# Optimization experiments

Measured on AMD Instinct MI355X. Metric: run time of the kernel, lower is better.

## Reference

```python
import jax, jax.numpy as jnp
import numpy as np

K = 9            # connections per output pixel
GA = 2           # global additional samples
RA = 2           # relative additional samples
VS = 4 + GA + RA # 2^rank neighbours + sampled
REGION = 12      # int(0.25 * 48) per spatial dim
MMULT = 0.1
MIN_SIGMA = 0.05
SIGMA_SCALE = 0.05
SIGMA_BOOST = 2.0


def setup_inputs() -> dict:
    key = jax.random.key(0)
    ks = jax.random.split(key, 8)
    b, cin, h, w = 8, 128, 48, 48
    cout = 256
    hidden = cin * 4

    def lin_init(k, fan_out, fan_in):
        bound = 1.0 / np.sqrt(fan_in)
        kw, kb = jax.random.split(k)
        W = jax.random.uniform(kw, (fan_out, fan_in), minval=-bound, maxval=bound, dtype=jnp.float32)
        bb = jax.random.uniform(kb, (fan_out,), minval=-bound, maxval=bound, dtype=jnp.float32)
        return W, bb

    x = jax.random.normal(ks[0], (b, cin, h, w), dtype=jnp.float32)
    W1, b1 = lin_init(ks[1], hidden, 2)          # toparams layer 1 (adaptive=False -> 2 coord inputs)
    W2, b2 = lin_init(ks[2], 3 * K, hidden)      # toparams layer 2 -> k means (2d) + k sigmas
    Wu, bu = lin_init(ks[3], cout, K * cin)      # unify linear
    gints = jax.random.randint(ks[4], (b, h, w, K, GA, 2), 0, h, dtype=jnp.int32)      # global samples (h==w)
    roff = jax.random.randint(ks[5], (b, h, w, K, RA, 2), 0, REGION, dtype=jnp.int32)  # relative offsets
    return {"x": x, "W1": W1, "b1": b1, "W2": W2, "b2": b2, "Wu": Wu, "bu": bu,
            "gints": gints, "roff": roff}


def reference(x, W1, b1, W2, b2, Wu, bu, gints, roff):
    b, c, h, w = x.shape
    s = jnp.array([h, w], dtype=x.dtype)                       # spatial range per dim
    s_int = jnp.array([h, w], dtype=jnp.int32)

    # normalized coordinate grid in [0,1], (h, w, 2) with [.,.,0]=row, [.,.,1]=col
    rows = jnp.arange(h, dtype=x.dtype) / (h - 1)
    cols = jnp.arange(w, dtype=x.dtype) / (w - 1)
    coords = jnp.stack(jnp.meshgrid(rows, cols, indexing='ij'), axis=-1)

    # hypernetwork: per-pixel coords -> K 2d mean offsets + K sigmas
    inp = jnp.broadcast_to(coords, (b, h, w, 2))
    hid = jax.nn.relu(inp @ W1.T + b1)
    params = hid @ W2.T + b2                                   # (b,h,w,3K)
    means_raw = params[..., :2 * K].reshape(b, h, w, K, 2)
    sig_raw = params[..., 2 * K:]                              # (b,h,w,K)

    # mids: inverse of the sigmoid scaling applied to the pixel's own coordinate
    pix = coords * (s - 1)                                     # pixel coordinates
    sc = pix / (s - 1) * 0.9999 + 0.00005
    mids = jnp.log(sc / (1.0 - sc))                            # (h,w,2)

    # transform_means: sigmoid -> [0, s-1]
    means = jax.nn.sigmoid(mids[None, :, :, None, :] + MMULT * means_raw) * (s - 1)  # (b,h,w,K,2)
    # transform_sigmas: softplus(. + boost) + min, per-dim scale, then sigma_scale
    sigmas = (jax.nn.softplus(sig_raw + SIGMA_BOOST) + MIN_SIGMA)[..., None] * s * SIGMA_SCALE  # (b,h,w,K,2)

    # ---- integer index generation (non-differentiable) ----
    fl = jnp.floor(jax.lax.stop_gradient(means)).astype(jnp.int32)   # (b,h,w,K,2)
    combos = jnp.array([[0, 0], [0, 1], [1, 0], [1, 1]], dtype=jnp.int32)
    neigh = fl[..., None, :] + combos                                 # (b,h,w,K,4,2)
    rel = fl[..., None, :] + roff - REGION // 2                       # (b,h,w,K,RA,2)
    ints = jnp.concatenate([neigh, gints, rel], axis=-2) % s_int      # (b,h,w,K,VS,2)

    # duplicate masking: zero any tuple that occurred earlier along VS
    eq = jnp.all(ints[..., :, None, :] == ints[..., None, :, :], axis=-1)  # (...,VS,VS)
    lower = jnp.tril(jnp.ones((VS, VS), dtype=bool), k=-1)
    dups = jnp.any(eq & lower, axis=-1)                               # (b,h,w,K,VS)

    # unnormalized gaussian densities of integer points under (means, sigmas)
    diff = (ints.astype(x.dtype) - means[..., None, :]) / sigmas[..., None, :]
    props = jnp.exp(-0.5 * jnp.sum(diff * diff, axis=-1))             # (b,h,w,K,VS)
    props = jnp.where(dups, jnp.zeros((), x.dtype), props)
    weights = props / jnp.sum(props, axis=-1, keepdims=True)          # mvalues are all-ones

    # irregular gather of input channel vectors at sampled pixels
    lin = ints[..., 0] * w + ints[..., 1]                             # (b,h,w,K,VS)
    flat = x.transpose(0, 2, 3, 1).reshape(b, h * w, c)
    feats = flat[jnp.arange(b)[:, None], lin.reshape(b, -1)]          # (b, h*w*K*VS, c)
    feats = feats.reshape(b, h, w, K, VS, c)

    feats = jnp.einsum('bhwkvc,bhwkv->bhwkc', feats, weights)         # weighted reduce over VS
    feats = feats.reshape(b, h, w, K * c)
    out = feats @ Wu.T + bu                                           # unify linear
    return out.transpose(0, 3, 1, 2)                                  # (b, cout, h, w)
```

## Files before the change

kernel.cpp:

```cpp
#include <hip/hip_runtime.h>
#include <hip/hip_bf16.h>
#include <hip/hip_fp16.h>

#define BB 8
#define CIN 128
#define HH 48
#define WW 48
#define HW 2304
#define KK 9
#define COUT 256
#define KC 1152
#define MM 18432
#define MT 32
#define SFP 136

#define LIGHT_BARRIER() asm volatile("s_waitcnt lgkmcnt(0)\n\ts_barrier" ::: "memory")

typedef short bf16x8_t __attribute__((ext_vector_type(8)));
typedef float f32x16_t __attribute__((ext_vector_type(16)));
typedef float f32x4_t  __attribute__((ext_vector_type(4)));

static __device__ __forceinline__ float b2f(short u) {
    union { unsigned int i; float f; } c;
    c.i = ((unsigned int)(unsigned short)u) << 16;
    return c.f;
}

__global__ __launch_bounds__(256) void prep_kernel(
    const float* __restrict__ x, __hip_bfloat16* __restrict__ xT,
    const float* __restrict__ Wu, bf16x8_t* __restrict__ Bp,
    const float* __restrict__ W1, const float* __restrict__ b1,
    const float* __restrict__ W2, const float* __restrict__ b2,
    float* __restrict__ means, float* __restrict__ sigmas, int* __restrict__ fls)
{
    int bid = blockIdx.x;
    int t = threadIdx.x;

    if (bid < 576) {
        __shared__ float tile[64][65];
        int ij0 = (bid % 36) * 64;
        int c0  = ((bid / 36) % 2) * 64;
        int b   = bid / 72;
        int ijl = t & 63, cl = t >> 6;
        #pragma unroll
        for (int i = 0; i < 16; i++) {
            int cc = i*4 + cl;
            tile[cc][ijl] = x[(size_t)(b*CIN + c0 + cc) * HW + ij0 + ijl];
        }
        __syncthreads();
        int cl2 = t & 63, ijl2 = t >> 6;
        #pragma unroll
        for (int i = 0; i < 16; i++) {
            int ij = i*4 + ijl2;
            xT[(size_t)(b*HW + ij0 + ij) * CIN + c0 + cl2] = __float2bfloat16(tile[cl2][ij]);
        }
    } else if (bid < 720) {
        int idx = (bid - 576) * 256 + t;
        int lane = idx & 63;
        int rest = idx >> 6;
        int s = rest % 72, g = rest / 72;
        int r = lane & 31, qq = lane >> 5;
        const float* src = Wu + (size_t)(g*32 + r) * KC + s*16 + qq*8;
        union { bf16x8_t v; __hip_bfloat16 h[8]; } o;
        #pragma unroll
        for (int j = 0; j < 8; j++) o.h[j] = __float2bfloat16(src[j]);
        Bp[idx] = o.v;
    } else {
        int wave = t >> 6, lane = t & 63;
        int p = (bid - 720) * 4 + wave;
        int iy = p / WW, ix = p % WW;
        float ryf = (float)iy / 47.0f;
        float rxf = (float)ix / 47.0f;
        double ry = (double)ryf, rx = (double)rxf;

        double h[8];
        #pragma unroll
        for (int jj = 0; jj < 8; jj++) {
            int j = lane*8 + jj;
            double v = ry * (double)W1[j*2+0] + rx * (double)W1[j*2+1] + (double)b1[j];
            h[jj] = v > 0.0 ? v : 0.0;
        }
        double par[27];
        #pragma unroll
        for (int o = 0; o < 27; o++) {
            const float4* w4 = (const float4*)(W2 + (size_t)o*512 + lane*8);
            float4 wa = w4[0], wb = w4[1];
            double s = (double)wa.x*h[0] + (double)wa.y*h[1]
                     + (double)wa.z*h[2] + (double)wa.w*h[3]
                     + (double)wb.x*h[4] + (double)wb.y*h[5]
                     + (double)wb.z*h[6] + (double)wb.w*h[7];
            par[o] = s;
        }
        #pragma unroll
        for (int o = 0; o < 27; o++) {
            #pragma unroll
            for (int d = 1; d < 64; d <<= 1)
                par[o] += __shfl_xor(par[o], d, 64);
            par[o] += (double)b2[o];
        }
        if (lane < KK) {
            int k = lane;
            double scy = ry * 0.9999 + 5e-05;
            double scx = rx * 0.9999 + 5e-05;
            double midy = log(scy / (1.0 - scy));
            double midx = log(scx / (1.0 - scx));
            double zy = midy + 0.1 * par[2*k+0];
            double zx = midx + 0.1 * par[2*k+1];
            double my = 47.0 / (1.0 + exp(-zy));
            double mx = 47.0 / (1.0 + exp(-zx));
            double sr = par[18 + k] + 2.0;
            double sp = (sr > 0.0 ? sr : 0.0) + log1p(exp(-fabs(sr)));
            double sg = (sp + 0.05) * 48.0 * 0.05;
            means[(p*KK + k)*2 + 0] = (float)my;
            means[(p*KK + k)*2 + 1] = (float)mx;
            sigmas[p*KK + k] = (float)sg;
            fls[(p*KK + k)*2 + 0] = (int)floor(my);
            fls[(p*KK + k)*2 + 1] = (int)floor(mx);
        }
    }
}

__global__ __launch_bounds__(512, 4) void fused_kernel(
    const float* __restrict__ means, const float* __restrict__ sigmas,
    const int* __restrict__ fls, const int* __restrict__ gints,
    const int* __restrict__ roff, const short* __restrict__ xT,
    const bf16x8_t* __restrict__ Bp, const float* __restrict__ bu,
    float* __restrict__ out)
{
    __shared__ unsigned int s_tap[KK*MT*8];
    __shared__ __align__(16) short s_feat[2][MT*SFP];

    int t = threadIdx.x;
    int b   = blockIdx.x & 7;
    int grp = blockIdx.x >> 3;
    int ij0 = grp * MT;
    int m0  = b * HW + ij0;

    if (t < KK*MT) {
        int p = t;
        int k = p >> 5, row = p & 31;
        int ij = ij0 + row;
        int bij = m0 + row;
        int fy = fls[(ij*KK + k)*2 + 0];
        int fx = fls[(ij*KK + k)*2 + 1];
        float my = means[(ij*KK + k)*2 + 0];
        float mx = means[(ij*KK + k)*2 + 1];
        float sg = sigmas[ij*KK + k];
        int lins[8]; float ws[8];
        #pragma unroll
        for (int v = 0; v < 8; v++) {
            int iy, ix;
            if (v < 4) {
                iy = fy + (v >> 1); ix = fx + (v & 1);
            } else if (v < 6) {
                int base = ((bij*KK + k)*2 + (v - 4)) * 2;
                iy = gints[base]; ix = gints[base + 1];
            } else {
                int base = ((bij*KK + k)*2 + (v - 6)) * 2;
                iy = fy + roff[base] - 6; ix = fx + roff[base + 1] - 6;
            }
            iy = ((iy % HH) + HH) % HH;
            ix = ((ix % WW) + WW) % WW;
            lins[v] = iy * WW + ix;
            float dy = ((float)iy - my) / sg;
            float dx = ((float)ix - mx) / sg;
            ws[v] = expf(-0.5f * (dy*dy + dx*dx));
        }
        #pragma unroll
        for (int v = 1; v < 8; v++) {
            bool dup = false;
            #pragma unroll
            for (int u = 0; u < 8; u++) if (u < v) dup = dup || (lins[u] == lins[v]);
            if (dup) ws[v] = 0.0f;
        }
        float sum = 0.0f;
        #pragma unroll
        for (int v = 0; v < 8; v++) sum += ws[v];
        float inv = 1.0f / sum;
        #pragma unroll
        for (int v = 0; v < 8; v++) {
            unsigned short hb = __half_as_ushort(__float2half(ws[v] * inv));
            s_tap[p*8+v] = ((unsigned int)lins[v] << 16) | (unsigned int)hb;
        }
    }
    LIGHT_BARRIER();

    const short* xb = xT + (size_t)b * (HW * CIN);
    int lane = t & 63, wave = t >> 6;
    int r = lane & 31, q = lane >> 5;
    int grow = t >> 4, gc0 = (t & 15) << 3;

    f32x16_t acc = {};

    for (int k = 0; k < KK; k++) {
        bf16x8_t tap[8];
        float    wgt[8];
        {
            const unsigned int* tp = &s_tap[(k*MT + grow)*8];
            #pragma unroll
            for (int v = 0; v < 8; v++) {
                unsigned int e = tp[v];
                wgt[v] = __half2float(__ushort_as_half((unsigned short)(e & 0xffffu)));
                tap[v] = *(const bf16x8_t*)(xb + (size_t)(e >> 16) * CIN + gc0);
            }
        }
        {
            float a0[8];
            #pragma unroll
            for (int j = 0; j < 8; j++) a0[j] = 0.0f;
            #pragma unroll
            for (int v = 0; v < 8; v++) {
                float w = wgt[v]; bf16x8_t d8 = tap[v];
                #pragma unroll
                for (int j = 0; j < 8; j++) a0[j] += w * b2f(d8[j]);
            }
            union { bf16x8_t v8; __hip_bfloat16 hh[8]; } o;
            #pragma unroll
            for (int j = 0; j < 8; j++) o.hh[j] = __float2bfloat16(a0[j]);
            *(bf16x8_t*)(&s_feat[k & 1][grow*SFP + gc0]) = o.v8;
        }
        LIGHT_BARRIER();
        {
            int base = (wave*72 + k*8)*64 + lane;
            const short* fb = s_feat[k & 1];
            #pragma unroll
            for (int si = 0; si < 8; si++) {
                bf16x8_t Bf = Bp[base + si*64];
                bf16x8_t a = *(const bf16x8_t*)(fb + r*SFP + si*16 + q*8);
                acc = __builtin_amdgcn_mfma_f32_32x32x16_bf16(a, Bf, acc, 0, 0, 0);
            }
        }
    }

    int n = wave*32 + r;
    float bv = bu[n];
    float* oc = out + ((size_t)b * COUT + n) * HW + ij0;
    #pragma unroll
    for (int g4 = 0; g4 < 4; g4++) {
        f32x4_t vv;
        vv[0] = acc[g4*4+0] + bv;
        vv[1] = acc[g4*4+1] + bv;
        vv[2] = acc[g4*4+2] + bv;
        vv[3] = acc[g4*4+3] + bv;
        *(f32x4_t*)(oc + g4*8 + q*4) = vv;
    }
}

extern "C" void kernel_launch(void* const* d_in, const int* in_sizes, int n_in,
                              void* d_out, int out_size, void* d_ws, size_t ws_size,
                              hipStream_t stream)
{
    const float* x   = (const float*)d_in[0];
    const float* W1  = (const float*)d_in[1];
    const float* b1  = (const float*)d_in[2];
    const float* W2  = (const float*)d_in[3];
    const float* b2  = (const float*)d_in[4];
    const float* Wu  = (const float*)d_in[5];
    const float* bu  = (const float*)d_in[6];
    const int* gints = (const int*)d_in[7];
    const int* roff  = (const int*)d_in[8];
    float* out = (float*)d_out;

    char* ws = (char*)d_ws;
    float* ws_means  = (float*)(ws + 0);
    float* ws_sigma  = (float*)(ws + 165888);
    int*   ws_fl     = (int*  )(ws + 248832);
    short* ws_xT     = (short*)(ws + 414720);
    bf16x8_t* ws_bp  = (bf16x8_t*)(ws + 5133312);

    prep_kernel<<<1296, 256, 0, stream>>>(x, (__hip_bfloat16*)ws_xT, Wu, ws_bp,
                                          W1, b1, W2, b2,
                                          ws_means, ws_sigma, ws_fl);
    fused_kernel<<<MM/MT, 512, 0, stream>>>(ws_means, ws_sigma, ws_fl, gints, roff,
                                            ws_xT, ws_bp, bu, out);
}
```

Measured before the change: 145.3 us.

## Gather two kernel taps per iteration across thread halves to halve barriers

The gather stage now splits the 512 threads into two halves, each building the weighted feature tile for a different tap k, so two taps are produced per loop iteration. Each thread handles 16 channels (two 16-byte loads per sample) instead of 8. The loop runs 5 times instead of 9, cutting block barriers roughly in half and raising the number of gather loads in flight per thread. The cost is double the shared-memory feature buffer, more registers per thread, and an odd final iteration in which half the threads sit idle.

Result: slower. 150.1 us (+3.3%).

```diff
diff --git a/kernel.cpp b/kernel.cpp
--- a/kernel.cpp
+++ b/kernel.cpp
@@ -13,6 +13,7 @@
 #define MM 18432
 #define MT 32
 #define SFP 136
+#define NP 5
 
 #define LIGHT_BARRIER() asm volatile("s_waitcnt lgkmcnt(0)\n\ts_barrier" ::: "memory")
 
@@ -128,7 +129,7 @@
     float* __restrict__ out)
 {
     __shared__ unsigned int s_tap[KK*MT*8];
-    __shared__ __align__(16) short s_feat[2][MT*SFP];
+    __shared__ __align__(16) short s_feat[2][2][MT*SFP];
 
     int t = threadIdx.x;
     int b   = blockIdx.x & 7;
@@ -188,46 +189,61 @@
     const short* xb = xT + (size_t)b * (HW * CIN);
     int lane = t & 63, wave = t >> 6;
     int r = lane & 31, q = lane >> 5;
-    int grow = t >> 4, gc0 = (t & 15) << 3;
+    int cpart = t >> 8;
+    int grow = (t >> 3) & 31;
+    int gc0 = (t & 7) << 4;
 
     f32x16_t acc = {};
 
-    for (int k = 0; k < KK; k++) {
-        bf16x8_t tap[8];
-        float    wgt[8];
-        {
-            const unsigned int* tp = &s_tap[(k*MT + grow)*8];
+    for (int p = 0; p < NP; p++) {
+        int kg = 2*p + cpart;
+        if (kg < KK) {
+            const unsigned int* tp = &s_tap[(kg*MT + grow)*8];
+            unsigned int e[8];
+            #pragma unroll
+            for (int v = 0; v < 8; v++) e[v] = tp[v];
+            bf16x8_t d0[8], d1[8];
             #pragma unroll
             for (int v = 0; v < 8; v++) {
-                unsigned int e = tp[v];
-                wgt[v] = __half2float(__ushort_as_half((unsigned short)(e & 0xffffu)));
-                tap[v] = *(const bf16x8_t*)(xb + (size_t)(e >> 16) * CIN + gc0);
-            }
-        }
-        {
-            float a0[8];
-            #pragma unroll
-            for (int j = 0; j < 8; j++) a0[j] = 0.0f;
+                const bf16x8_t* sp = (const bf16x8_t*)(xb + (size_t)(e[v] >> 16) * CIN + gc0);
+                d0[v] = sp[0];
+                d1[v] = sp[1];
+            }
+            float a0[16];
+            #pragma unroll
+            for (int j = 0; j < 16; j++) a0[j] = 0.0f;
             #pragma unroll
             for (int v = 0; v < 8; v++) {
-                float w = wgt[v]; bf16x8_t d8 = tap[v];
+                float w = __half2float(__ushort_as_half((unsigned short)(e[v] & 0xffffu)));
                 #pragma unroll
-                for (int j = 0; j < 8; j++) a0[j] += w * b2f(d8[j]);
-            }
-            union { bf16x8_t v8; __hip_bfloat16 hh[8]; } o;
-            #pragma unroll
-            for (int j = 0; j < 8; j++) o.hh[j] = __float2bfloat16(a0[j]);
-            *(bf16x8_t*)(&s_feat[k & 1][grow*SFP + gc0]) = o.v8;
+                for (int j = 0; j < 8; j++) {
+                    a0[j]   += w * b2f(d0[v][j]);
+                    a0[8+j] += w * b2f(d1[v][j]);
+                }
+            }
+            union { bf16x8_t v8; __hip_bfloat16 hh[8]; } o0, o1;
+            #pragma unroll
+            for (int j = 0; j < 8; j++) {
+                o0.hh[j] = __float2bfloat16(a0[j]);
+                o1.hh[j] = __float2bfloat16(a0[8+j]);
+            }
+            bf16x8_t* fd = (bf16x8_t*)(&s_feat[p & 1][cpart][grow*SFP + gc0]);
+            fd[0] = o0.v8;
+            fd[1] = o1.v8;
         }
         LIGHT_BARRIER();
-        {
-            int base = (wave*72 + k*8)*64 + lane;
-            const short* fb = s_feat[k & 1];
-            #pragma unroll
-            for (int si = 0; si < 8; si++) {
-                bf16x8_t Bf = Bp[base + si*64];
-                bf16x8_t a = *(const bf16x8_t*)(fb + r*SFP + si*16 + q*8);
-                acc = __builtin_amdgcn_mfma_f32_32x32x16_bf16(a, Bf, acc, 0, 0, 0);
+        #pragma unroll
+        for (int cc = 0; cc < 2; cc++) {
+            int k = 2*p + cc;
+            if (k < KK) {
+                const short* fb = s_feat[p & 1][cc];
+                int base = (wave*72 + k*8)*64 + lane;
+                #pragma unroll
+                for (int si = 0; si < 8; si++) {
+                    bf16x8_t Bf = Bp[base + si*64];
+                    bf16x8_t a = *(const bf16x8_t*)(fb + r*SFP + si*16 + q*8);
+                    acc = __builtin_amdgcn_mfma_f32_32x32x16_bf16(a, Bf, acc, 0, 0, 0);
+                }
             }
         }
     }
```

## Warp-specialize fused kernel into gather producers and MFMA consumers with LDS flags

Applied to the files above, without the earlier changes.

Splits the block into 8 gather waves that build per-tap weighted feature tiles and 4 MFMA waves that each handle two 32-column output slices. Shared-memory counters with a triple-buffered feature tile replace the per-tap block barriers, so gathers for later taps can overlap the matrix multiply of earlier ones. The block grows to 768 threads and each consumer wave holds two accumulators, which raises register pressure and adds spin-wait overhead. The launch bound (768, 6) may also not fit the requested occupancy.

Measured after the change: 147.6 us. Within noise of the previous version (+1.6%).

```diff
diff --git a/kernel.cpp b/kernel.cpp
--- a/kernel.cpp
+++ b/kernel.cpp
@@ -13,8 +13,6 @@
 #define MM 18432
 #define MT 32
 #define SFP 136
-
-#define LIGHT_BARRIER() asm volatile("s_waitcnt lgkmcnt(0)\n\ts_barrier" ::: "memory")
 
 typedef short bf16x8_t __attribute__((ext_vector_type(8)));
 typedef float f32x16_t __attribute__((ext_vector_type(16)));
@@ -120,7 +118,7 @@
     }
 }
 
-__global__ __launch_bounds__(512, 4) void fused_kernel(
+__global__ __launch_bounds__(768, 6) void fused_kernel(
     const float* __restrict__ means, const float* __restrict__ sigmas,
     const int* __restrict__ fls, const int* __restrict__ gints,
     const int* __restrict__ roff, const short* __restrict__ xT,
@@ -128,13 +126,17 @@
     float* __restrict__ out)
 {
     __shared__ unsigned int s_tap[KK*MT*8];
-    __shared__ __align__(16) short s_feat[2][MT*SFP];
+    __shared__ __align__(16) short s_feat[3][MT*SFP];
+    __shared__ int s_ready[KK];
+    __shared__ int s_done[KK];
 
     int t = threadIdx.x;
     int b   = blockIdx.x & 7;
     int grp = blockIdx.x >> 3;
     int ij0 = grp * MT;
     int m0  = b * HW + ij0;
+
+    if (t < KK) { s_ready[t] = 0; s_done[t] = 0; }
 
     if (t < KK*MT) {
         int p = t;
@@ -183,66 +185,85 @@
             s_tap[p*8+v] = ((unsigned int)lins[v] << 16) | (unsigned int)hb;
         }
     }
-    LIGHT_BARRIER();
-
-    const short* xb = xT + (size_t)b * (HW * CIN);
+    __syncthreads();
+
     int lane = t & 63, wave = t >> 6;
-    int r = lane & 31, q = lane >> 5;
-    int grow = t >> 4, gc0 = (t & 15) << 3;
-
-    f32x16_t acc = {};
-
-    for (int k = 0; k < KK; k++) {
-        bf16x8_t tap[8];
-        float    wgt[8];
-        {
+
+    if (wave < 8) {
+        const short* xb = xT + (size_t)b * (HW * CIN);
+        int grow = t >> 4, gc0 = (t & 15) << 3;
+        for (int k = 0; k < KK; k++) {
+            if (k >= 3) {
+                while (__hip_atomic_load(&s_done[k-3], __ATOMIC_ACQUIRE,
+                                         __HIP_MEMORY_SCOPE_WORKGROUP) < 4)
+                    __builtin_amdgcn_s_sleep(1);
+            }
             const unsigned int* tp = &s_tap[(k*MT + grow)*8];
+            unsigned int e[8];
+            #pragma unroll
+            for (int v = 0; v < 8; v++) e[v] = tp[v];
+            bf16x8_t tap[8];
+            #pragma unroll
+            for (int v = 0; v < 8; v++)
+                tap[v] = *(const bf16x8_t*)(xb + (size_t)(e[v] >> 16) * CIN + gc0);
+            float a0[8];
+            #pragma unroll
+            for (int j = 0; j < 8; j++) a0[j] = 0.0f;
             #pragma unroll
             for (int v = 0; v < 8; v++) {
-                unsigned int e = tp[v];
-                wgt[v] = __half2float(__ushort_as_half((unsigned short)(e & 0xffffu)));
-                tap[v] = *(const bf16x8_t*)(xb + (size_t)(e >> 16) * CIN + gc0);
-            }
-        }
-        {
-            float a0[8];
-            #pragma unroll
-            for (int j = 0; j < 8; j++) a0[j] = 0.0f;
-            #pragma unroll
-            for (int v = 0; v < 8; v++) {
-                float w = wgt[v]; bf16x8_t d8 = tap[v];
+                float w = __half2float(__ushort_as_half((unsigned short)(e[v] & 0xffffu)));
+                bf16x8_t d8 = tap[v];
                 #pragma unroll
                 for (int j = 0; j < 8; j++) a0[j] += w * b2f(d8[j]);
             }
             union { bf16x8_t v8; __hip_bfloat16 hh[8]; } o;
             #pragma unroll
             for (int j = 0; j < 8; j++) o.hh[j] = __float2bfloat16(a0[j]);
-            *(bf16x8_t*)(&s_feat[k & 1][grow*SFP + gc0]) = o.v8;
-        }
-        LIGHT_BARRIER();
-        {
-            int base = (wave*72 + k*8)*64 + lane;
-            const short* fb = s_feat[k & 1];
-            #pragma unroll
-            for (int si = 0; si < 8; si++) {
-                bf16x8_t Bf = Bp[base + si*64];
-                bf16x8_t a = *(const bf16x8_t*)(fb + r*SFP + si*16 + q*8);
-                acc = __builtin_amdgcn_mfma_f32_32x32x16_bf16(a, Bf, acc, 0, 0, 0);
-            }
-        }
-    }
-
-    int n = wave*32 + r;
-    float bv = bu[n];
-    float* oc = out + ((size_t)b * COUT + n) * HW + ij0;
-    #pragma unroll
-    for (int g4 = 0; g4 < 4; g4++) {
-        f32x4_t vv;
-        vv[0] = acc[g4*4+0] + bv;
-        vv[1] = acc[g4*4+1] + bv;
-        vv[2] = acc[g4*4+2] + bv;
-        vv[3] = acc[g4*4+3] + bv;
-        *(f32x4_t*)(oc + g4*8 + q*4) = vv;
+            *(bf16x8_t*)(&s_feat[k % 3][grow*SFP + gc0]) = o.v8;
+            asm volatile("s_waitcnt lgkmcnt(0)" ::: "memory");
+            if (lane == 0)
+                __hip_atomic_fetch_add(&s_ready[k], 1, __ATOMIC_RELEASE,
+                                       __HIP_MEMORY_SCOPE_WORKGROUP);
+        }
+    } else {
+        int cw = wave - 8;
+        int r = lane & 31, q = lane >> 5;
+        f32x16_t acc[2] = {};
+        for (int k = 0; k < KK; k++) {
+            while (__hip_atomic_load(&s_ready[k], __ATOMIC_ACQUIRE,
+                                     __HIP_MEMORY_SCOPE_WORKGROUP) < 8)
+                __builtin_amdgcn_s_sleep(1);
+            const short* fb = s_feat[k % 3];
+            #pragma unroll
+            for (int h = 0; h < 2; h++) {
+                int base = ((cw*2 + h)*72 + k*8)*64 + lane;
+                #pragma unroll
+                for (int si = 0; si < 8; si++) {
+                    bf16x8_t Bf = Bp[base + si*64];
+                    bf16x8_t a = *(const bf16x8_t*)(fb + r*SFP + si*16 + q*8);
+                    acc[h] = __builtin_amdgcn_mfma_f32_32x32x16_bf16(a, Bf, acc[h], 0, 0, 0);
+                }
+            }
+            asm volatile("s_waitcnt lgkmcnt(0)" ::: "memory");
+            if (lane == 0)
+                __hip_atomic_fetch_add(&s_done[k], 1, __ATOMIC_RELEASE,
+                                       __HIP_MEMORY_SCOPE_WORKGROUP);
+        }
+        #pragma unroll
+        for (int h = 0; h < 2; h++) {
+            int n = cw*64 + h*32 + r;
+            float bv = bu[n];
+            float* oc = out + ((size_t)b * COUT + n) * HW + ij0;
+            #pragma unroll
+            for (int g4 = 0; g4 < 4; g4++) {
+                f32x4_t vv;
+                vv[0] = acc[h][g4*4+0] + bv;
+                vv[1] = acc[h][g4*4+1] + bv;
+                vv[2] = acc[h][g4*4+2] + bv;
+                vv[3] = acc[h][g4*4+3] + bv;
+                *(f32x4_t*)(oc + g4*8 + q*4) = vv;
+            }
+        }
     }
 }
 
@@ -271,6 +292,6 @@
     prep_kernel<<<1296, 256, 0, stream>>>(x, (__hip_bfloat16*)ws_xT, Wu, ws_bp,
                                           W1, b1, W2, b2,
                                           ws_means, ws_sigma, ws_fl);
-    fused_kernel<<<MM/MT, 512, 0, stream>>>(ws_means, ws_sigma, ws_fl, gints, roff,
+    fused_kernel<<<MM/MT, 768, 0, stream>>>(ws_means, ws_sigma, ws_fl, gints, roff,
                                             ws_xT, ws_bp, bu, out);
 }
```
